# Optimization experiments

Measured on AMD Instinct MI355X. Metric: run time of the kernel, lower is better.

## Reference

```python
import jax, jax.numpy as jnp
import numpy as np

BG_ID = 0
RADIUS = 10
MODE = 'gauss'
LAMBDA_B = 1.0
GAMMA = 0.1
TEMP = 4.0
EPS = 1e-8
BIG = 1e6  # stands in for +inf (no fg in a row/column); BIG**2 is fp32-safe


def setup_inputs() -> dict:
    key = jax.random.key(0)
    k1, k2 = jax.random.split(key)
    B, C, H, W = 4, 19, 256, 256
    return {
        'student_logits': jax.random.normal(k1, (B, C, H, W), jnp.float32),
        'teacher_logits': jax.random.normal(k2, (B, C, H, W), jnp.float32),
    }


def _edt2(fg):
    """Exact squared Euclidean distance transform of (1 - fg):
    distance from each pixel to the nearest foreground pixel.
    Separable algorithm: 1D column pass (two cumulative scans), then
    exact lower-envelope minimization along rows (vectorized brute force).
    fg: bool [B, H, W]. Returns float32 [B, H, W]."""
    B, H, W = fg.shape
    ii = jnp.arange(H, dtype=jnp.float32)[None, :, None]  # row index
    # 1D vertical distance to nearest fg pixel in each column
    d_fwd = ii - jax.lax.cummax(jnp.where(fg, ii, -BIG), axis=1)
    d_bwd = -jax.lax.cummax(jnp.where(fg, -ii, -BIG), axis=1, reverse=True) - ii
    g = jnp.minimum(jnp.minimum(d_fwd, d_bwd), BIG)  # [B,H,W]
    # exact 2D squared EDT: dist2[b,i,j] = min_{j'} (j-j')^2 + g[b,i,j']^2
    jj = jnp.arange(W, dtype=jnp.float32)
    diff2 = (jj[:, None] - jj[None, :]) ** 2  # [W, W']
    dist2 = jnp.min(diff2[None, None, :, :] + (g * g)[:, :, None, :], axis=-1)
    return dist2


def _erode(fg):
    """scipy.ndimage.binary_erosion with 4-connected cross structure and
    border_value=0 (out-of-bounds treated as background)."""
    p = jnp.pad(fg, ((0, 0), (1, 1), (1, 1)))
    return fg & p[:, :-2, 1:-1] & p[:, 2:, 1:-1] & p[:, 1:-1, :-2] & p[:, 1:-1, 2:]


def _weight_map(teacher_logits):
    # argmax of softmax(probs) == argmax of logits (softmax is monotone per-pixel)
    pred = jnp.argmax(teacher_logits, axis=1)  # [B,H,W]
    fg = pred != BG_ID
    dist2 = _edt2(fg)
    dist = jnp.sqrt(dist2)
    mask = (dist <= RADIUS).astype(jnp.float32)
    sigma = RADIUS / 2.0
    if MODE == 'gauss':
        wdist = jnp.exp(-dist2 / (2.0 * sigma * sigma))
    else:
        wdist = jnp.clip(1.0 - dist / RADIUS, 0.0, 1.0)
    wdist = wdist * mask
    boundary = (fg & ~_erode(fg)).astype(jnp.float32)
    # wb = wdist*(1+lambda_b*boundary); final weights = wb*mask_inside
    # (if an image has no fg pixels, dist is huge -> mask==0 -> weights==0,
    #  matching the scipy loop's `continue` which leaves zeros)
    return wdist * (1.0 + LAMBDA_B * boundary) * mask


def reference(student_logits, teacher_logits):
    weight_map = _weight_map(teacher_logits)  # [B,H,W]
    # teacher probs at temperature T (torch computes t_prob_T and t_prob
    # identically twice; computed once here)
    t_prob = jax.nn.softmax(teacher_logits / TEMP, axis=1)
    entropy = -jnp.sum(t_prob * jnp.log(jnp.clip(t_prob, EPS, None)), axis=1)
    ent_max = jnp.max(entropy, axis=(1, 2), keepdims=True)
    conf_factor = GAMMA + (1.0 - GAMMA) * (1.0 - entropy / (ent_max + EPS))
    s_logp = jax.nn.log_softmax(student_logits / TEMP, axis=1)
    kl_per_pixel = jnp.sum(t_prob * (jnp.log(t_prob + EPS) - s_logp), axis=1)
    total_weight = weight_map * conf_factor
    loss = jnp.sum(total_weight * kl_per_pixel) / (jnp.sum(total_weight) + EPS)
    return TEMP * TEMP * loss
```

## Files before the change

kernel.cpp:

```cpp
#include <hip/hip_runtime.h>
#include <math.h>

#define NC   19
#define HH   256
#define WW   256
#define NB   4
#define HW   (HH * WW)
#define NPIX (NB * HW)
#define RAD  10
#define CAP2 121.0f

__global__ __launch_bounds__(256) void k_pixel(
    const float* __restrict__ student, const float* __restrict__ teacher,
    float* __restrict__ entropy, float* __restrict__ kl,
    unsigned char* __restrict__ fg, unsigned int* __restrict__ entmax)
{
    int q = (blockIdx.x * 256 + threadIdx.x) * 2;
    int b = q >> 16;
    int r = q & (HW - 1);
    const float* tb = teacher + (size_t)b * NC * HW + r;
    const float* sb = student + (size_t)b * NC * HW + r;

    float2 t[NC], s[NC];
    float tmx = -INFINITY, tmy = -INFINITY, smx = -INFINITY, smy = -INFINITY;
    int ax = 0, ay = 0;
#pragma unroll
    for (int c = 0; c < NC; ++c) {
        t[c] = *(const float2*)(tb + (size_t)c * HW);
        s[c] = *(const float2*)(sb + (size_t)c * HW);
        if (t[c].x > tmx) { tmx = t[c].x; ax = c; }
        if (t[c].y > tmy) { tmy = t[c].y; ay = c; }
        smx = fmaxf(smx, s[c].x);
        smy = fmaxf(smy, s[c].y);
    }
    float Stx = 0.f, Sty = 0.f, Ssx = 0.f, Ssy = 0.f;
#pragma unroll
    for (int c = 0; c < NC; ++c) {
        Stx += expf((t[c].x - tmx) * 0.25f);
        Sty += expf((t[c].y - tmy) * 0.25f);
        Ssx += expf((s[c].x - smx) * 0.25f);
        Ssy += expf((s[c].y - smy) * 0.25f);
    }
    float lStx = logf(Stx), lSty = logf(Sty);
    float lSsx = logf(Ssx), lSsy = logf(Ssy);
    const float LEPS = -18.420681f;
    float entx = 0.f, enty = 0.f, klx = 0.f, kly = 0.f;
#pragma unroll
    for (int c = 0; c < NC; ++c) {
        float lpx = (t[c].x - tmx) * 0.25f - lStx;
        float lpy = (t[c].y - tmy) * 0.25f - lSty;
        float pcx = expf(lpx), pcy = expf(lpy);
        entx -= pcx * fmaxf(lpx, LEPS);
        enty -= pcy * fmaxf(lpy, LEPS);
        float slpx = (s[c].x - smx) * 0.25f - lSsx;
        float slpy = (s[c].y - smy) * 0.25f - lSsy;
        klx += pcx * (logf(pcx + 1e-8f) - slpx);
        kly += pcy * (logf(pcy + 1e-8f) - slpy);
    }
    *(float2*)(entropy + q) = make_float2(entx, enty);
    *(float2*)(kl + q)      = make_float2(klx, kly);
    fg[q]     = (ax != 0) ? 1 : 0;
    fg[q + 1] = (ay != 0) ? 1 : 0;

    float m = fmaxf(entx, enty);
#pragma unroll
    for (int o = 32; o >= 1; o >>= 1) m = fmaxf(m, __shfl_down(m, o, 64));
    __shared__ float smem[4];
    int wave = threadIdx.x >> 6, lane = threadIdx.x & 63;
    if (lane == 0) smem[wave] = m;
    __syncthreads();
    if (threadIdx.x == 0) {
        m = fmaxf(fmaxf(smem[0], smem[1]), fmaxf(smem[2], smem[3]));
        atomicMax(entmax + b, __float_as_uint(m));
    }
}

#define TS   32
#define HALO 10
#define FW   (TS + 2 * HALO)

__global__ __launch_bounds__(256) void k_tile(
    const unsigned char* __restrict__ fg, const float* __restrict__ entropy,
    const float* __restrict__ kl, const unsigned int* __restrict__ entmax,
    double* __restrict__ acc)
{
    __shared__ unsigned char fgt[FW][FW];
    __shared__ float vm[TS][FW];
    int b   = blockIdx.z;
    int ti0 = blockIdx.y * TS;
    int tj0 = blockIdx.x * TS;
    int tid = threadIdx.x;
    const unsigned char* fgb = fg + (size_t)b * HW;

    for (int l = tid; l < FW * FW; l += 256) {
        int li = l / FW, lj = l - li * FW;
        int gi = ti0 - HALO + li, gj = tj0 - HALO + lj;
        unsigned char v = 0;
        if (gi >= 0 && gi < HH && gj >= 0 && gj < WW) v = fgb[gi * WW + gj];
        fgt[li][lj] = v;
    }
    __syncthreads();

    for (int l = tid; l < TS * FW; l += 256) {
        int i = l / FW, j = l - i * FW;
        float m = CAP2;
#pragma unroll
        for (int di = -HALO; di <= HALO; ++di)
            if (fgt[i + HALO + di][j]) m = fminf(m, (float)(di * di));
        vm[i][j] = m;
    }
    __syncthreads();

    float em = __uint_as_float(entmax[b]);
    double num = 0.0, den = 0.0;
#pragma unroll
    for (int k = 0; k < (TS * TS) / 256; ++k) {
        int p = tid + k * 256;
        int i = p >> 5, j = p & (TS - 1);
        float d2 = CAP2;
#pragma unroll
        for (int dj = -HALO; dj <= HALO; ++dj)
            d2 = fminf(d2, (float)(dj * dj) + vm[i][j + HALO + dj]);
        float mask  = (d2 <= 100.0f) ? 1.0f : 0.0f;
        float wdist = expf(-d2 * 0.02f) * mask;

        int f  = fgt[i + HALO][j + HALO];
        int up = fgt[i + HALO - 1][j + HALO];
        int dn = fgt[i + HALO + 1][j + HALO];
        int lf = fgt[i + HALO][j + HALO - 1];
        int rt = fgt[i + HALO][j + HALO + 1];
        float boundary = (f && !(up && dn && lf && rt)) ? 1.0f : 0.0f;

        float w = wdist * (1.0f + boundary) * mask;
        size_t gidx = (size_t)b * HW + (size_t)(ti0 + i) * WW + (tj0 + j);
        float conf = 0.1f + 0.9f * (1.0f - entropy[gidx] / (em + 1e-8f));
        float tw = w * conf;
        num += (double)(tw * kl[gidx]);
        den += (double)tw;
    }

#pragma unroll
    for (int o = 32; o >= 1; o >>= 1) {
        num += __shfl_down(num, o, 64);
        den += __shfl_down(den, o, 64);
    }
    __shared__ double snum[4], sden[4];
    int wave = tid >> 6, lane = tid & 63;
    if (lane == 0) { snum[wave] = num; sden[wave] = den; }
    __syncthreads();
    if (tid == 0) {
        atomicAdd(acc + 0, snum[0] + snum[1] + snum[2] + snum[3]);
        atomicAdd(acc + 1, sden[0] + sden[1] + sden[2] + sden[3]);
    }
}

__global__ void k_out(const double* __restrict__ acc, float* __restrict__ out)
{
    out[0] = (float)(16.0 * acc[0] / (acc[1] + 1e-8));
}

extern "C" void kernel_launch(void* const* d_in, const int* in_sizes, int n_in,
                              void* d_out, int out_size, void* d_ws, size_t ws_size,
                              hipStream_t stream)
{
    const float* student = (const float*)d_in[0];
    const float* teacher = (const float*)d_in[1];
    float* out = (float*)d_out;

    char* ws = (char*)d_ws;
    double*        acc     = (double*)(ws + 0);
    unsigned int*  entmax  = (unsigned int*)(ws + 64);
    float*         entropy = (float*)(ws + 128);
    float*         kl      = (float*)(ws + 128 + (size_t)NPIX * 4);
    unsigned char* fg      = (unsigned char*)(ws + 128 + (size_t)NPIX * 8);

    hipMemsetAsync(ws, 0, 128, stream);

    k_pixel<<<NPIX / 2 / 256, 256, 0, stream>>>(student, teacher, entropy, kl, fg, entmax);
    dim3 g2(WW / TS, HH / TS, NB);
    k_tile<<<g2, 256, 0, stream>>>(fg, entropy, kl, entmax, acc);
    k_out<<<1, 1, 0, stream>>>(acc, out);
}
```

Before: 102.1 us.

## Use closed-form entropy/KL, fast intrinsics, and fuse launches with last-block finalize

Replaces the second per-channel pass, with its expf and two logf calls per channel, by closed-form entropy and KL built from weighted sums (sum p*t, sum p*s) and one log per softmax. This drops the epsilon clamping, so results can differ slightly. The memset, the float atomicMax and the separate k_out launch are removed: k_pixel zeroes the accumulators and writes per-block maxima, k_tile reduces those maxima, and the last block to finish writes the output. Shared fg tiles are stored as floats so the vertical pass and the boundary test become branchless min operations. The risks are fp rounding differences from the algebraic rewrite and fast intrinsics, and relying on stream ordering for the accumulator reset done inside k_pixel.

```diff
diff --git a/kernel.cpp b/kernel.cpp
--- a/kernel.cpp
+++ b/kernel.cpp
@@ -13,8 +13,12 @@
 __global__ __launch_bounds__(256) void k_pixel(
     const float* __restrict__ student, const float* __restrict__ teacher,
     float* __restrict__ entropy, float* __restrict__ kl,
-    unsigned char* __restrict__ fg, unsigned int* __restrict__ entmax)
+    unsigned char* __restrict__ fg, float* __restrict__ bmax,
+    double* __restrict__ acc, unsigned int* __restrict__ done)
 {
+    if (blockIdx.x == 0 && threadIdx.x == 0) {
+        acc[0] = 0.0; acc[1] = 0.0; *done = 0u;
+    }
     int q = (blockIdx.x * 256 + threadIdx.x) * 2;
     int b = q >> 16;
     int r = q & (HW - 1);
@@ -34,33 +38,27 @@
         smy = fmaxf(smy, s[c].y);
     }
     float Stx = 0.f, Sty = 0.f, Ssx = 0.f, Ssy = 0.f;
+    float T1x = 0.f, T1y = 0.f, T2x = 0.f, T2y = 0.f;
 #pragma unroll
     for (int c = 0; c < NC; ++c) {
-        Stx += expf((t[c].x - tmx) * 0.25f);
-        Sty += expf((t[c].y - tmy) * 0.25f);
-        Ssx += expf((s[c].x - smx) * 0.25f);
-        Ssy += expf((s[c].y - smy) * 0.25f);
+        float ex = __expf((t[c].x - tmx) * 0.25f);
+        float ey = __expf((t[c].y - tmy) * 0.25f);
+        Stx += ex;            Sty += ey;
+        T1x += ex * t[c].x;   T1y += ey * t[c].y;
+        T2x += ex * s[c].x;   T2y += ey * s[c].y;
+        Ssx += __expf((s[c].x - smx) * 0.25f);
+        Ssy += __expf((s[c].y - smy) * 0.25f);
     }
-    float lStx = logf(Stx), lSty = logf(Sty);
-    float lSsx = logf(Ssx), lSsy = logf(Ssy);
-    const float LEPS = -18.420681f;
-    float entx = 0.f, enty = 0.f, klx = 0.f, kly = 0.f;
-#pragma unroll
-    for (int c = 0; c < NC; ++c) {
-        float lpx = (t[c].x - tmx) * 0.25f - lStx;
-        float lpy = (t[c].y - tmy) * 0.25f - lSty;
-        float pcx = expf(lpx), pcy = expf(lpy);
-        entx -= pcx * fmaxf(lpx, LEPS);
-        enty -= pcy * fmaxf(lpy, LEPS);
-        float slpx = (s[c].x - smx) * 0.25f - lSsx;
-        float slpy = (s[c].y - smy) * 0.25f - lSsy;
-        klx += pcx * (logf(pcx + 1e-8f) - slpx);
-        kly += pcy * (logf(pcy + 1e-8f) - slpy);
-    }
+    float rStx = 1.0f / Stx, rSty = 1.0f / Sty;
+    float entx = (tmx - T1x * rStx) * 0.25f + __logf(Stx);
+    float enty = (tmy - T1y * rSty) * 0.25f + __logf(Sty);
+    float klx = -entx - ((T2x * rStx - smx) * 0.25f - __logf(Ssx));
+    float kly = -enty - ((T2y * rSty - smy) * 0.25f - __logf(Ssy));
+
     *(float2*)(entropy + q) = make_float2(entx, enty);
     *(float2*)(kl + q)      = make_float2(klx, kly);
-    fg[q]     = (ax != 0) ? 1 : 0;
-    fg[q + 1] = (ay != 0) ? 1 : 0;
+    uchar2 fgv = make_uchar2((ax != 0) ? 1 : 0, (ay != 0) ? 1 : 0);
+    *(uchar2*)(fg + q) = fgv;
 
     float m = fmaxf(entx, enty);
 #pragma unroll
@@ -69,10 +67,8 @@
     int wave = threadIdx.x >> 6, lane = threadIdx.x & 63;
     if (lane == 0) smem[wave] = m;
     __syncthreads();
-    if (threadIdx.x == 0) {
-        m = fmaxf(fmaxf(smem[0], smem[1]), fmaxf(smem[2], smem[3]));
-        atomicMax(entmax + b, __float_as_uint(m));
-    }
+    if (threadIdx.x == 0)
+        bmax[blockIdx.x] = fmaxf(fmaxf(smem[0], smem[1]), fmaxf(smem[2], smem[3]));
 }
 
 #define TS   32
@@ -81,37 +77,47 @@
 
 __global__ __launch_bounds__(256) void k_tile(
     const unsigned char* __restrict__ fg, const float* __restrict__ entropy,
-    const float* __restrict__ kl, const unsigned int* __restrict__ entmax,
-    double* __restrict__ acc)
+    const float* __restrict__ kl, const float* __restrict__ bmax,
+    double* __restrict__ acc, unsigned int* __restrict__ done,
+    float* __restrict__ out)
 {
-    __shared__ unsigned char fgt[FW][FW];
+    __shared__ float fgt[FW][FW];
     __shared__ float vm[TS][FW];
+    __shared__ float wmax[4];
     int b   = blockIdx.z;
     int ti0 = blockIdx.y * TS;
     int tj0 = blockIdx.x * TS;
     int tid = threadIdx.x;
+    int wave = tid >> 6, lane = tid & 63;
     const unsigned char* fgb = fg + (size_t)b * HW;
+
+    float m = bmax[b * 128 + (tid & 127)];
+#pragma unroll
+    for (int o = 32; o >= 1; o >>= 1) m = fmaxf(m, __shfl_down(m, o, 64));
+    if (lane == 0) wmax[wave] = m;
 
     for (int l = tid; l < FW * FW; l += 256) {
         int li = l / FW, lj = l - li * FW;
         int gi = ti0 - HALO + li, gj = tj0 - HALO + lj;
-        unsigned char v = 0;
-        if (gi >= 0 && gi < HH && gj >= 0 && gj < WW) v = fgb[gi * WW + gj];
+        float v = 0.f;
+        if (gi >= 0 && gi < HH && gj >= 0 && gj < WW) v = (float)fgb[gi * WW + gj];
         fgt[li][lj] = v;
     }
     __syncthreads();
+    float em = fmaxf(fmaxf(wmax[0], wmax[1]), fmaxf(wmax[2], wmax[3]));
 
     for (int l = tid; l < TS * FW; l += 256) {
         int i = l / FW, j = l - i * FW;
-        float m = CAP2;
+        float mn = CAP2;
 #pragma unroll
-        for (int di = -HALO; di <= HALO; ++di)
-            if (fgt[i + HALO + di][j]) m = fminf(m, (float)(di * di));
-        vm[i][j] = m;
+        for (int di = -HALO; di <= HALO; ++di) {
+            float fv = fgt[i + HALO + di][j];
+            mn = fminf(mn, (float)(di * di) + (1.0f - fv) * 1000.0f);
+        }
+        vm[i][j] = mn;
     }
     __syncthreads();
 
-    float em = __uint_as_float(entmax[b]);
     double num = 0.0, den = 0.0;
 #pragma unroll
     for (int k = 0; k < (TS * TS) / 256; ++k) {
@@ -122,14 +128,12 @@
         for (int dj = -HALO; dj <= HALO; ++dj)
             d2 = fminf(d2, (float)(dj * dj) + vm[i][j + HALO + dj]);
         float mask  = (d2 <= 100.0f) ? 1.0f : 0.0f;
-        float wdist = expf(-d2 * 0.02f) * mask;
+        float wdist = __expf(-d2 * 0.02f) * mask;
 
-        int f  = fgt[i + HALO][j + HALO];
-        int up = fgt[i + HALO - 1][j + HALO];
-        int dn = fgt[i + HALO + 1][j + HALO];
-        int lf = fgt[i + HALO][j + HALO - 1];
-        int rt = fgt[i + HALO][j + HALO + 1];
-        float boundary = (f && !(up && dn && lf && rt)) ? 1.0f : 0.0f;
+        float f  = fgt[i + HALO][j + HALO];
+        float mn4 = fminf(fminf(fgt[i + HALO - 1][j + HALO], fgt[i + HALO + 1][j + HALO]),
+                          fminf(fgt[i + HALO][j + HALO - 1], fgt[i + HALO][j + HALO + 1]));
+        float boundary = (f != 0.f && mn4 == 0.f) ? 1.0f : 0.0f;
 
         float w = wdist * (1.0f + boundary) * mask;
         size_t gidx = (size_t)b * HW + (size_t)(ti0 + i) * WW + (tj0 + j);
@@ -145,18 +149,19 @@
         den += __shfl_down(den, o, 64);
     }
     __shared__ double snum[4], sden[4];
-    int wave = tid >> 6, lane = tid & 63;
     if (lane == 0) { snum[wave] = num; sden[wave] = den; }
     __syncthreads();
     if (tid == 0) {
         atomicAdd(acc + 0, snum[0] + snum[1] + snum[2] + snum[3]);
         atomicAdd(acc + 1, sden[0] + sden[1] + sden[2] + sden[3]);
+        __threadfence();
+        unsigned int old = atomicAdd(done, 1u);
+        if (old == (gridDim.x * gridDim.y * gridDim.z - 1)) {
+            double tn = atomicAdd(acc + 0, 0.0);
+            double td = atomicAdd(acc + 1, 0.0);
+            out[0] = (float)(16.0 * tn / (td + 1e-8));
+        }
     }
-}
-
-__global__ void k_out(const double* __restrict__ acc, float* __restrict__ out)
-{
-    out[0] = (float)(16.0 * acc[0] / (acc[1] + 1e-8));
 }
 
 extern "C" void kernel_launch(void* const* d_in, const int* in_sizes, int n_in,
@@ -169,15 +174,14 @@
 
     char* ws = (char*)d_ws;
     double*        acc     = (double*)(ws + 0);
-    unsigned int*  entmax  = (unsigned int*)(ws + 64);
-    float*         entropy = (float*)(ws + 128);
-    float*         kl      = (float*)(ws + 128 + (size_t)NPIX * 4);
-    unsigned char* fg      = (unsigned char*)(ws + 128 + (size_t)NPIX * 8);
+    unsigned int*  done    = (unsigned int*)(ws + 16);
+    float*         bmax    = (float*)(ws + 64);
+    float*         entropy = (float*)(ws + 4096);
+    float*         kl      = (float*)(ws + 4096 + (size_t)NPIX * 4);
+    unsigned char* fg      = (unsigned char*)(ws + 4096 + (size_t)NPIX * 8);
 
-    hipMemsetAsync(ws, 0, 128, stream);
-
-    k_pixel<<<NPIX / 2 / 256, 256, 0, stream>>>(student, teacher, entropy, kl, fg, entmax);
+    k_pixel<<<NPIX / 2 / 256, 256, 0, stream>>>(student, teacher, entropy, kl,
+                                                fg, bmax, acc, done);
     dim3 g2(WW / TS, HH / TS, NB);
-    k_tile<<<g2, 256, 0, stream>>>(fg, entropy, kl, entmax, acc);
-    k_out<<<1, 1, 0, stream>>>(acc, out);
+    k_tile<<<g2, 256, 0, stream>>>(fg, entropy, kl, bmax, acc, done, out);
 }
```

Result: faster. 94.21 us (-7.7%).
